# Optimization experiments

Measured on AMD Instinct MI355X. Metric: run time of the kernel, lower is better.

Reference implementation:

```python
import jax, jax.numpy as jnp
import numpy as np
from jax import lax

IN_FEATURES = 1024
CLASSES = 512
OUT_CHANNELS = 32
N = 4096
CONV1_OUT = 32
K = 3


def setup_inputs() -> dict:
    key = jax.random.key(0)
    ks = jax.random.split(key, 7)
    s_lin = 1.0 / np.sqrt(IN_FEATURES)
    s_c1 = 1.0 / np.sqrt(1 * K)
    s_c2 = 1.0 / np.sqrt(CONV1_OUT * K)
    return {
        "x": jax.random.normal(ks[0], (N, IN_FEATURES), dtype=jnp.float32),
        "W_w": jax.random.uniform(ks[1], (CLASSES, IN_FEATURES), jnp.float32, -s_lin, s_lin),
        "W_b": jax.random.uniform(ks[2], (CLASSES,), jnp.float32, -s_lin, s_lin),
        "conv1_w": jax.random.uniform(ks[3], (CONV1_OUT, 1, K), jnp.float32, -s_c1, s_c1),
        "conv1_b": jax.random.uniform(ks[4], (CONV1_OUT,), jnp.float32, -s_c1, s_c1),
        "conv2_w": jax.random.uniform(ks[5], (OUT_CHANNELS, CONV1_OUT, K), jnp.float32, -s_c2, s_c2),
        "conv2_b": jax.random.uniform(ks[6], (OUT_CHANNELS,), jnp.float32, -s_c2, s_c2),
    }


def _conv1d(x, w, b):
    # x: [N, C_in, L], w: [C_out, C_in, K], padding=1 (same)
    y = lax.conv_general_dilated(
        x, w, window_strides=(1,), padding=((1, 1),),
        dimension_numbers=("NCH", "OIH", "NCH"))
    return y + b[None, :, None]


def reference(x, W_w, W_b, conv1_w, conv1_b, conv2_w, conv2_b):
    # SelfAttention: h = x W^T + b  -> [N, CLASSES]
    h = x @ W_w.T + W_b
    # attention = softmax(tanh(h h^T), dim=1)  -> [N, N]
    scores = jnp.tanh(h @ h.T)
    attn = jax.nn.softmax(scores, axis=1)
    a = jnp.tanh(attn @ h)                     # [N, CLASSES]
    a = jax.nn.relu(a)
    # unsqueeze(-1).permute(0,2,1): [N, CLASSES] -> [N, 1, CLASSES]
    z = a[:, None, :]
    z = jax.nn.relu(_conv1d(z, conv1_w, conv1_b))   # [N, 32, CLASSES]
    z = jax.nn.relu(_conv1d(z, conv2_w, conv2_b))   # [N, OUT_CHANNELS, CLASSES]
    return jnp.transpose(z, (0, 2, 1))              # [N, CLASSES, OUT_CHANNELS]
```

## Files before the change

### kernel.cpp

```cpp
#include <hip/hip_runtime.h>

typedef __bf16 bf16_t;
typedef __bf16 bf16x8 __attribute__((ext_vector_type(8)));
typedef __bf16 bf16x4v __attribute__((ext_vector_type(4)));
typedef __bf16 bf16x2 __attribute__((ext_vector_type(2)));
typedef float f32x4 __attribute__((ext_vector_type(4)));

__device__ __forceinline__ float tanh_fast(float x) {
  float a = fabsf(x);
  float e = __expf(-2.f * a);
  float t = (1.f - e) / (1.f + e);
  return copysignf(t, x);
}

__device__ __forceinline__ void gload16(const void* g, void* l) {
  __builtin_amdgcn_global_load_lds(
      (const __attribute__((address_space(1))) void*)g,
      (__attribute__((address_space(3))) void*)l, 16, 0, 0);
}

__global__ __launch_bounds__(256) void cast_all_k(const float* __restrict__ x,
                                                  const float* __restrict__ Ww,
                                                  const float* __restrict__ w2,
                                                  bf16_t* __restrict__ xb,
                                                  bf16_t* __restrict__ Wbf,
                                                  bf16_t* __restrict__ w2rg) {
  const int bid = blockIdx.x;
  const int tid = threadIdx.x;
  if (bid < 4096) {
    const int i = bid * 256 + tid;
    float4 v = ((const float4*)x)[i];
    bf16x4v o;
    o[0] = (bf16_t)v.x; o[1] = (bf16_t)v.y; o[2] = (bf16_t)v.z; o[3] = (bf16_t)v.w;
    ((bf16x4v*)xb)[i] = o;
  } else if (bid < 4608) {
    const int i = (bid - 4096) * 256 + tid;
    float4 v = ((const float4*)Ww)[i];
    bf16x4v o;
    o[0] = (bf16_t)v.x; o[1] = (bf16_t)v.y; o[2] = (bf16_t)v.z; o[3] = (bf16_t)v.w;
    ((bf16x4v*)Wbf)[i] = o;
  } else {
    for (int i = tid; i < 3072; i += 256) {
      int o = i / 96, rem = i % 96, c = rem / 3, kk = rem % 3;
      w2rg[kk * 1024 + o * 32 + c] = (bf16_t)w2[i];
    }
  }
}

#define BAR() __builtin_amdgcn_s_barrier()
#define WLG() asm volatile("s_waitcnt lgkmcnt(0)" ::: "memory")
#define RDA(b, am)                                                              \
  do {                                                                          \
    _Pragma("unroll") for (int j = 0; j < 4; ++j) {                             \
      afr[j][0] = *(const bf16x8*)(pA + (b)*16384 + (am)*4096 + j*1024);        \
      afr[j][1] = *(const bf16x8*)(pA + (b)*16384 + 8192 + (am)*4096 + j*1024); \
    }                                                                           \
  } while (0)
#define RDB(b, bn)                                                              \
  do {                                                                          \
    _Pragma("unroll") for (int jj = 0; jj < 2; ++jj) {                          \
      bfr[jj][0] = *(const bf16x8*)(pB + (b)*16384 + ((bn)*2+jj)*1024);         \
      bfr[jj][1] = *(const bf16x8*)(pB + (b)*16384 + 8192 + ((bn)*2+jj)*1024);  \
    }                                                                           \
  } while (0)
#define MM16(am, bn)                                                            \
  do {                                                                          \
    __builtin_amdgcn_s_setprio(1);                                              \
    _Pragma("unroll") for (int kk = 0; kk < 2; ++kk)                            \
    _Pragma("unroll") for (int j = 0; j < 4; ++j)                               \
    _Pragma("unroll") for (int jj = 0; jj < 2; ++jj)                            \
      acc[(am)*4+j][(bn)*2+jj] = __builtin_amdgcn_mfma_f32_16x16x32_bf16(       \
          afr[j][kk], bfr[jj][kk], acc[(am)*4+j][(bn)*2+jj], 0, 0, 0);          \
    __builtin_amdgcn_s_setprio(0);                                              \
  } while (0)
#define STGA(tile, half)                                                        \
  do {                                                                          \
    const bf16_t* s_ = Ag + (size_t)(half)*128*lda + (tile)*64;                 \
    char* d_ = lds_raw + (half)*32768 + ((tile)&1)*16384 + tid*16;              \
    gload16(s_, d_); gload16(s_ + 32, d_ + 8192);                               \
  } while (0)
#define STGB(tile, half)                                                        \
  do {                                                                          \
    const bf16_t* s_ = Bg + (size_t)(half)*128*ldb + (tile)*64;                 \
    char* d_ = lds_raw + 65536 + (half)*32768 + ((tile)&1)*16384 + tid*16;      \
    gload16(s_, d_); gload16(s_ + 32, d_ + 8192);                               \
  } while (0)

template <int EPI>
__global__ __launch_bounds__(512, 2) void gemm8_k(const bf16_t* __restrict__ A,
                                                  const bf16_t* __restrict__ Bt,
                                                  bf16_t* __restrict__ out,
                                                  float* __restrict__ psum,
                                                  int lda, int ldb, int ldc,
                                                  int Klen, size_t pstride) {
  __shared__ __attribute__((aligned(16))) char lds_raw[131072];
  const int tid = threadIdx.x;
  const int wid = tid >> 6, l = tid & 63;
  const int wm = wid >> 2, wn = wid & 3;
  const int lr = l & 15, lkq = l >> 4;
  const int bx = blockIdx.x, by = blockIdx.y;
  const size_t koff = (size_t)blockIdx.z * Klen;
  const int NI = Klen >> 7;

  const int srow = tid >> 2;
  const int scol = ((tid & 3) * 8) ^ (((tid >> 5) & 1) << 4);
  const bf16_t* Ag = A + (size_t)(by * 256 + srow) * lda + koff + scol;
  const bf16_t* Bg = Bt + (size_t)(bx * 256 + srow) * ldb + koff + scol;

  const int kby = (lkq * 16) ^ (((lr >> 3) & 1) << 5);
  const char* pA = lds_raw + wm * 32768 + lr * 64 + kby;
  const char* pB = lds_raw + 65536 + (wn >> 1) * 32768 + ((wn & 1) * 64 + lr) * 64 + kby;

  bf16x8 afr[4][2], bfr[2][2];
  f32x4 acc[8][4];
#pragma unroll
  for (int m = 0; m < 8; ++m)
#pragma unroll
    for (int n = 0; n < 4; ++n) acc[m][n] = (f32x4){0.f, 0.f, 0.f, 0.f};

  STGA(0, 0); STGA(0, 1); STGB(0, 0); STGB(0, 1); STGA(1, 0);

  for (int i = 0; i < NI; ++i) {
    const int t1 = 2 * i + 1, t2 = 2 * i + 2, t3 = 2 * i + 3;
    const bool more = (i + 1 < NI);
    asm volatile("s_waitcnt vmcnt(2)" ::: "memory");
    BAR();
    RDA(0, 0); RDB(0, 0);
    STGA(t1, 1);
    WLG(); MM16(0, 0); BAR();
    RDB(0, 1); STGB(t1, 0);
    BAR(); WLG(); MM16(0, 1); BAR();
    RDA(0, 1); STGB(t1, 1);
    BAR(); WLG(); MM16(1, 1); BAR();
    RDB(0, 0);
    if (more) STGA(t2, 0);
    BAR(); WLG(); MM16(1, 0); BAR();
    if (more) { asm volatile("s_waitcnt vmcnt(2)" ::: "memory"); }
    else      { asm volatile("s_waitcnt vmcnt(0)" ::: "memory"); }
    BAR();
    RDA(1, 0); RDB(1, 0);
    if (more) STGA(t2, 1);
    WLG(); MM16(0, 0); BAR();
    RDB(1, 1);
    if (more) STGB(t2, 0);
    BAR(); WLG(); MM16(0, 1); BAR();
    RDA(1, 1);
    if (more) STGB(t2, 1);
    BAR(); WLG(); MM16(1, 1); BAR();
    RDB(1, 0);
    if (more) STGA(t3, 0);
    BAR(); WLG(); MM16(1, 0); BAR();
  }

  if constexpr (EPI == 1) {
    float* ps = psum + (size_t)(bx * 4 + wn) * 4096;
#pragma unroll
    for (int mi = 0; mi < 8; ++mi) {
#pragma unroll
      for (int v = 0; v < 4; ++v) {
        const int row = by * 256 + wm * 128 + mi * 16 + lkq * 4 + v;
        float rs = 0.f;
#pragma unroll
        for (int ni = 0; ni < 4; ++ni) {
          const int col = bx * 256 + wn * 64 + ni * 16 + lr;
          float val = __expf(tanh_fast(acc[mi][ni][v]));
          out[(size_t)row * ldc + col] = (bf16_t)val;
          rs += val;
        }
        rs += __shfl_xor(rs, 1);
        rs += __shfl_xor(rs, 2);
        rs += __shfl_xor(rs, 4);
        rs += __shfl_xor(rs, 8);
        if (lr == 0) ps[row] = rs;
      }
    }
  } else {
    bf16_t* o = out + (size_t)blockIdx.z * pstride;
#pragma unroll
    for (int mi = 0; mi < 8; ++mi)
#pragma unroll
      for (int v = 0; v < 4; ++v) {
        const int row = by * 256 + wm * 128 + mi * 16 + lkq * 4 + v;
#pragma unroll
        for (int ni = 0; ni < 4; ++ni)
          o[(size_t)row * ldc + bx * 256 + wn * 64 + ni * 16 + lr] = (bf16_t)acc[mi][ni][v];
      }
  }
}

template <int EPI>
__global__ __launch_bounds__(256) void gemm_bt_k(const bf16_t* __restrict__ A,
                                                 const bf16_t* __restrict__ Bt,
                                                 const float* __restrict__ extra,
                                                 bf16_t* __restrict__ out,
                                                 float* __restrict__ outf,
                                                 float* __restrict__ psum,
                                                 int M, int N, int Kloop, int lda, int ldb) {
  __shared__ bf16_t As[128 * 32];
  __shared__ bf16_t Bs[128 * 32];
  const int tid = threadIdx.x;
  const int w = tid >> 6;
  const int l = tid & 63;
  const int bx = blockIdx.x, by = blockIdx.y;
  const int koff = blockIdx.z * Kloop;

  const bf16_t* src = (w < 2) ? A : Bt;
  const int stride = (w < 2) ? lda : ldb;
  bf16_t* dstbase = (w < 2) ? As : Bs;
  const int tile0 = (w < 2 ? by : bx) * 128 + (w & 1) * 64;
  const int srow = l >> 2;
  const int scol = (l & 3) * 8;
  const bf16_t* gbase = src + (size_t)(tile0 + srow) * stride + scol + koff;
  bf16_t* lbase = dstbase + (w & 1) * (64 * 32);

  const int wm = w >> 1, wn = w & 1;
  const int lrow = l & 15;
  const int lk = (l >> 4) * 8;

  f32x4 zero = {0.f, 0.f, 0.f, 0.f};
  f32x4 acc[4][4];
  for (int m = 0; m < 4; ++m)
    for (int n = 0; n < 4; ++n) acc[m][n] = zero;

  for (int kt = 0; kt < Kloop; kt += 32) {
    const bf16_t* g = gbase + kt;
#pragma unroll
    for (int i = 0; i < 4; ++i) gload16(g + (size_t)i * 16 * stride, lbase + i * 512);
    __syncthreads();
    bf16x8 af[4], bfv[4];
#pragma unroll
    for (int m = 0; m < 4; ++m)
      af[m] = *(const bf16x8*)&As[(wm * 64 + m * 16 + lrow) * 32 + lk];
#pragma unroll
    for (int n = 0; n < 4; ++n)
      bfv[n] = *(const bf16x8*)&Bs[(wn * 64 + n * 16 + lrow) * 32 + lk];
#pragma unroll
    for (int m = 0; m < 4; ++m)
#pragma unroll
      for (int n = 0; n < 4; ++n)
        acc[m][n] = __builtin_amdgcn_mfma_f32_16x16x32_bf16(af[m], bfv[n], acc[m][n], 0, 0, 0);
    __syncthreads();
  }

  const int row0 = by * 128 + wm * 64;
  const int col0 = bx * 128 + wn * 64;

  if constexpr (EPI == 3) {
    float* of = outf + (size_t)blockIdx.z * M * N;
#pragma unroll
    for (int m = 0; m < 4; ++m)
#pragma unroll
      for (int v = 0; v < 4; ++v) {
        const int row = row0 + m * 16 + ((l >> 4) << 2) + v;
#pragma unroll
        for (int n = 0; n < 4; ++n)
          of[(size_t)row * N + col0 + n * 16 + lrow] = acc[m][n][v];
      }
    return;
  }

  if constexpr (EPI == 1) {
#pragma unroll
    for (int m = 0; m < 4; ++m)
#pragma unroll
      for (int v = 0; v < 4; ++v) {
        const int row = row0 + m * 16 + ((l >> 4) << 2) + v;
        float rs = 0.f;
#pragma unroll
        for (int n = 0; n < 4; ++n) {
          const int col = col0 + n * 16 + lrow;
          float val = __expf(tanh_fast(acc[m][n][v]));
          out[(size_t)row * N + col] = (bf16_t)val;
          rs += val;
        }
        if (psum) {
          rs += __shfl_xor(rs, 1);
          rs += __shfl_xor(rs, 2);
          rs += __shfl_xor(rs, 4);
          rs += __shfl_xor(rs, 8);
          if ((l & 15) == 0) psum[(size_t)(bx * 2 + wn) * M + row] = rs;
        }
      }
    return;
  }

  float bcol[4];
#pragma unroll
  for (int n = 0; n < 4; ++n)
    bcol[n] = (EPI == 0) ? extra[col0 + n * 16 + lrow] : 0.f;

#pragma unroll
  for (int m = 0; m < 4; ++m) {
#pragma unroll
    for (int v = 0; v < 4; ++v) {
      const int row = row0 + m * 16 + ((l >> 4) << 2) + v;
      float inv_dn = 1.f;
      if constexpr (EPI == 2) inv_dn = 1.f / extra[row];
#pragma unroll
      for (int n = 0; n < 4; ++n) {
        const int col = col0 + n * 16 + lrow;
        float val = acc[m][n][v];
        float o;
        if constexpr (EPI == 0) o = val + bcol[n];
        else o = fmaxf(tanh_fast(val * inv_dn), 0.f);
        out[(size_t)row * N + col] = (bf16_t)o;
      }
    }
  }
}

__global__ __launch_bounds__(256) void reduce1T_k(const float* __restrict__ p0,
                                                  const float* __restrict__ p1,
                                                  const float* __restrict__ bias,
                                                  bf16_t* __restrict__ h,
                                                  bf16_t* __restrict__ hT) {
  __shared__ bf16_t tile[64][65];
  const int d0 = blockIdx.x * 64;
  const int i0 = blockIdx.y * 64;
  const int tid = threadIdx.x;
#pragma unroll
  for (int p = 0; p < 2; ++p) {
    const int r = p * 32 + (tid >> 3);
    const int c8 = (tid & 7) * 8;
    const size_t idx = (size_t)(i0 + r) * 512 + d0 + c8;
    float4 a0 = *(const float4*)&p0[idx];
    float4 a1 = *(const float4*)&p0[idx + 4];
    float4 b0 = *(const float4*)&p1[idx];
    float4 b1 = *(const float4*)&p1[idx + 4];
    float4 w0 = *(const float4*)&bias[d0 + c8];
    float4 w1 = *(const float4*)&bias[d0 + c8 + 4];
    bf16x8 o;
    o[0] = (bf16_t)(a0.x + b0.x + w0.x);
    o[1] = (bf16_t)(a0.y + b0.y + w0.y);
    o[2] = (bf16_t)(a0.z + b0.z + w0.z);
    o[3] = (bf16_t)(a0.w + b0.w + w0.w);
    o[4] = (bf16_t)(a1.x + b1.x + w1.x);
    o[5] = (bf16_t)(a1.y + b1.y + w1.y);
    o[6] = (bf16_t)(a1.z + b1.z + w1.z);
    o[7] = (bf16_t)(a1.w + b1.w + w1.w);
    *(bf16x8*)&h[idx] = o;
#pragma unroll
    for (int k = 0; k < 8; ++k) tile[r][c8 + k] = o[k];
  }
  __syncthreads();
#pragma unroll
  for (int p = 0; p < 2; ++p) {
    const int d = p * 32 + (tid >> 3);
    const int i8 = (tid & 7) * 8;
    bf16x8 u;
#pragma unroll
    for (int k = 0; k < 8; ++k) u[k] = tile[i8 + k][d];
    *(bf16x8*)&hT[(size_t)(d0 + d) * 4096 + i0 + i8] = u;
  }
}

__global__ __launch_bounds__(256) void transpose_k(const bf16_t* __restrict__ h,
                                                   bf16_t* __restrict__ hT) {
  __shared__ bf16_t tile[64][65];
  const int i0 = blockIdx.x * 64;
  const int d0 = blockIdx.y * 64;
  const int tid = threadIdx.x;
#pragma unroll
  for (int p = 0; p < 2; ++p) {
    int r = p * 32 + (tid >> 3);
    int c8 = (tid & 7) * 8;
    bf16x8 v = *(const bf16x8*)&h[(size_t)(i0 + r) * 512 + d0 + c8];
#pragma unroll
    for (int k = 0; k < 8; ++k) tile[r][c8 + k] = v[k];
  }
  __syncthreads();
#pragma unroll
  for (int p = 0; p < 2; ++p) {
    int d = p * 32 + (tid >> 3);
    int i8 = (tid & 7) * 8;
    bf16x8 u;
#pragma unroll
    for (int k = 0; k < 8; ++k) u[k] = tile[i8 + k][d];
    *(bf16x8*)&hT[(size_t)(d0 + d) * 4096 + i0 + i8] = u;
  }
}

__global__ __launch_bounds__(256) void rowsum_k(const bf16_t* __restrict__ P,
                                                float* __restrict__ den) {
  const int r = blockIdx.x;
  const int tid = threadIdx.x;
  const bf16_t* p = P + (size_t)r * 4096 + tid * 16;
  bf16x8 a = *(const bf16x8*)p;
  bf16x8 b = *(const bf16x8*)(p + 8);
  float s = 0.f;
#pragma unroll
  for (int k = 0; k < 8; ++k) s += (float)a[k] + (float)b[k];
  __shared__ float red[256];
  red[tid] = s;
  __syncthreads();
  for (int off = 128; off > 0; off >>= 1) {
    if (tid < off) red[tid] += red[tid + off];
    __syncthreads();
  }
  if (tid == 0) den[r] = red[0];
}

__global__ __launch_bounds__(256) void conv2_fused_k(const bf16_t* __restrict__ pg,
                                                     const float* __restrict__ psum,
                                                     const bf16_t* __restrict__ w2rg,
                                                     const float* __restrict__ w1,
                                                     const float* __restrict__ b1,
                                                     const float* __restrict__ b2,
                                                     float* __restrict__ out, int S) {
  __shared__ bf16_t trow[516];
  __shared__ bf16_t z1t[514 * 40];
  __shared__ bf16_t w2r[3072];
  __shared__ float w1s[96], b1s[32], b2s[32];
  __shared__ float den_s;
  const int r = blockIdx.x;
  const int tid = threadIdx.x;

  if (tid < 96) w1s[tid] = w1[tid];
  if (tid < 32) { b1s[tid] = b1[tid]; b2s[tid] = b2[tid]; }
  ((bf16x8*)w2r)[tid] = ((const bf16x8*)w2rg)[tid];
  if (tid < 128) ((bf16x8*)w2r)[256 + tid] = ((const bf16x8*)w2rg)[256 + tid];

  if (tid < 64) {
    float dp = psum[(size_t)tid * 4096 + r];
    dp += __shfl_xor(dp, 32);
    dp += __shfl_xor(dp, 16);
    dp += __shfl_xor(dp, 8);
    dp += __shfl_xor(dp, 4);
    dp += __shfl_xor(dp, 2);
    dp += __shfl_xor(dp, 1);
    if (tid == 0) den_s = dp;
  }

  float a0 = 0.f, a1 = 0.f;
  {
    const bf16_t* pr = pg + (size_t)r * 512 + tid * 2;
    for (int z = 0; z < S; ++z) {
      bf16x2 v = *(const bf16x2*)(pr + (size_t)z * (4096 * 512));
      a0 += (float)v[0];
      a1 += (float)v[1];
    }
  }
  if (tid == 0) { trow[0] = (bf16_t)0.f; trow[513] = (bf16_t)0.f; }
  if (tid < 40) { z1t[tid] = (bf16_t)0.f; z1t[513 * 40 + tid] = (bf16_t)0.f; }
  __syncthreads();

  {
    const float inv = 1.f / den_s;
    trow[1 + 2 * tid] = (bf16_t)fmaxf(tanh_fast(a0 * inv), 0.f);
    trow[2 + 2 * tid] = (bf16_t)fmaxf(tanh_fast(a1 * inv), 0.f);
  }
  __syncthreads();

  {
    const int c = tid & 31;
    const int jb = (tid >> 5) * 64;
    const float wc0 = w1s[c * 3], wc1 = w1s[c * 3 + 1], wc2 = w1s[c * 3 + 2];
    const float bb = b1s[c];
    float tm = (float)trow[jb];
    float t0 = (float)trow[jb + 1];
    for (int j = jb; j < jb + 64; ++j) {
      float tp2 = (float)trow[j + 2];
      float v = fmaxf(bb + wc0 * tm + wc1 * t0 + wc2 * tp2, 0.f);
      z1t[(j + 1) * 40 + c] = (bf16_t)v;
      tm = t0; t0 = tp2;
    }
  }
  __syncthreads();

  const int w = tid >> 6, l = tid & 63;
  const int lrow = l & 15;
  const int lk = (l >> 4) * 8;
  bf16x8 af[3][2];
#pragma unroll
  for (int kk = 0; kk < 3; ++kk)
#pragma unroll
    for (int m = 0; m < 2; ++m)
      af[kk][m] = *(const bf16x8*)&w2r[kk * 1024 + (m * 16 + lrow) * 32 + lk];

  f32x4 zero = {0.f, 0.f, 0.f, 0.f};
  f32x4 acc[2][8];
#pragma unroll
  for (int m = 0; m < 2; ++m)
#pragma unroll
    for (int n = 0; n < 8; ++n) acc[m][n] = zero;

  const int j0 = w * 128;
#pragma unroll
  for (int kk = 0; kk < 3; ++kk) {
#pragma unroll
    for (int n = 0; n < 8; ++n) {
      bf16x8 bfv = *(const bf16x8*)&z1t[(j0 + n * 16 + lrow + kk) * 40 + lk];
      acc[0][n] = __builtin_amdgcn_mfma_f32_16x16x32_bf16(af[kk][0], bfv, acc[0][n], 0, 0, 0);
      acc[1][n] = __builtin_amdgcn_mfma_f32_16x16x32_bf16(af[kk][1], bfv, acc[1][n], 0, 0, 0);
    }
  }

#pragma unroll
  for (int m = 0; m < 2; ++m) {
    const int ob = m * 16 + ((l >> 4) << 2);
    const float bb0 = b2s[ob], bb1 = b2s[ob + 1], bb2 = b2s[ob + 2], bb3 = b2s[ob + 3];
#pragma unroll
    for (int n = 0; n < 8; ++n) {
      const int j = j0 + n * 16 + lrow;
      f32x4 res;
      res[0] = fmaxf(acc[m][n][0] + bb0, 0.f);
      res[1] = fmaxf(acc[m][n][1] + bb1, 0.f);
      res[2] = fmaxf(acc[m][n][2] + bb2, 0.f);
      res[3] = fmaxf(acc[m][n][3] + bb3, 0.f);
      *(f32x4*)&out[((size_t)r * 512 + j) * 32 + ob] = res;
    }
  }
}

__global__ __launch_bounds__(256) void conv_fused_k(const bf16_t* __restrict__ t,
                                                    const float* __restrict__ w1,
                                                    const float* __restrict__ b1,
                                                    const float* __restrict__ w2,
                                                    const float* __restrict__ b2,
                                                    float* __restrict__ out) {
  __shared__ bf16_t trow[516];
  __shared__ bf16_t z1t[514 * 40];
  __shared__ bf16_t w2r[3 * 32 * 32];
  __shared__ float w1s[96], b1s[32], b2s[32];
  const int r = blockIdx.x;
  const int tid = threadIdx.x;

  if (tid < 96) w1s[tid] = w1[tid];
  if (tid < 32) { b1s[tid] = b1[tid]; b2s[tid] = b2[tid]; }
  for (int i = tid; i < 3072; i += 256) {
    int o = i / 96, rem = i % 96, c = rem / 3, kk = rem % 3;
    w2r[kk * 1024 + o * 32 + c] = (bf16_t)w2[i];
  }
  {
    const bf16_t* tp = t + (size_t)r * 512;
    trow[1 + tid] = tp[tid];
    trow[1 + 256 + tid] = tp[256 + tid];
    if (tid == 0) { trow[0] = (bf16_t)0.f; trow[513] = (bf16_t)0.f; }
    if (tid < 40) { z1t[tid] = (bf16_t)0.f; z1t[513 * 40 + tid] = (bf16_t)0.f; }
  }
  __syncthreads();

  {
    const int c = tid & 31;
    const int jb = (tid >> 5) * 64;
    const float wc0 = w1s[c * 3], wc1 = w1s[c * 3 + 1], wc2 = w1s[c * 3 + 2];
    const float bb = b1s[c];
    float tm = (float)trow[jb];
    float t0 = (float)trow[jb + 1];
    for (int j = jb; j < jb + 64; ++j) {
      float tp2 = (float)trow[j + 2];
      float v = fmaxf(bb + wc0 * tm + wc1 * t0 + wc2 * tp2, 0.f);
      z1t[(j + 1) * 40 + c] = (bf16_t)v;
      tm = t0; t0 = tp2;
    }
  }
  __syncthreads();

  const int w = tid >> 6, l = tid & 63;
  const int lrow = l & 15;
  const int lk = (l >> 4) * 8;
  bf16x8 af[3][2];
#pragma unroll
  for (int kk = 0; kk < 3; ++kk)
#pragma unroll
    for (int m = 0; m < 2; ++m)
      af[kk][m] = *(const bf16x8*)&w2r[kk * 1024 + (m * 16 + lrow) * 32 + lk];

  f32x4 zero = {0.f, 0.f, 0.f, 0.f};
  f32x4 acc[2][8];
#pragma unroll
  for (int m = 0; m < 2; ++m)
#pragma unroll
    for (int n = 0; n < 8; ++n) acc[m][n] = zero;

  const int j0 = w * 128;
#pragma unroll
  for (int kk = 0; kk < 3; ++kk) {
#pragma unroll
    for (int n = 0; n < 8; ++n) {
      bf16x8 bfv = *(const bf16x8*)&z1t[(j0 + n * 16 + lrow + kk) * 40 + lk];
      acc[0][n] = __builtin_amdgcn_mfma_f32_16x16x32_bf16(af[kk][0], bfv, acc[0][n], 0, 0, 0);
      acc[1][n] = __builtin_amdgcn_mfma_f32_16x16x32_bf16(af[kk][1], bfv, acc[1][n], 0, 0, 0);
    }
  }

#pragma unroll
  for (int m = 0; m < 2; ++m) {
    const int ob = m * 16 + ((l >> 4) << 2);
    const float bb0 = b2s[ob], bb1 = b2s[ob + 1], bb2 = b2s[ob + 2], bb3 = b2s[ob + 3];
#pragma unroll
    for (int n = 0; n < 8; ++n) {
      const int j = j0 + n * 16 + lrow;
      f32x4 res;
      res[0] = fmaxf(acc[m][n][0] + bb0, 0.f);
      res[1] = fmaxf(acc[m][n][1] + bb1, 0.f);
      res[2] = fmaxf(acc[m][n][2] + bb2, 0.f);
      res[3] = fmaxf(acc[m][n][3] + bb3, 0.f);
      *(f32x4*)&out[((size_t)r * 512 + j) * 32 + ob] = res;
    }
  }
}

extern "C" void kernel_launch(void* const* d_in, const int* in_sizes, int n_in,
                              void* d_out, int out_size, void* d_ws, size_t ws_size,
                              hipStream_t stream) {
  const float* x = (const float*)d_in[0];
  const float* Ww = (const float*)d_in[1];
  const float* Wb = (const float*)d_in[2];
  const float* c1w = (const float*)d_in[3];
  const float* c1b = (const float*)d_in[4];
  const float* c2w = (const float*)d_in[5];
  const float* c2b = (const float*)d_in[6];
  float* out = (float*)d_out;
  char* ws = (char*)d_ws;

  bf16_t* xb  = (bf16_t*)(ws + 0);
  bf16_t* Wbf = (bf16_t*)(ws + 8388608);
  bf16_t* h   = (bf16_t*)(ws + 9437184);
  bf16_t* hT  = (bf16_t*)(ws + 13631488);
  bf16_t* tb  = (bf16_t*)(ws + 17825792);
  bf16_t* w2rg = (bf16_t*)(ws + 17825792);
  float*  den = (float*)(ws + 22020096);

  cast_all_k<<<4609, 256, 0, stream>>>(x, Ww, c2w, xb, Wbf, w2rg);

  const size_t NEED_FAST = 73416704ull;
  if (ws_size >= NEED_FAST) {
    float*  psum = (float*)(ws + 22036480);
    bf16_t* P    = (bf16_t*)(ws + 23085056);
    float*  pg1  = (float*)(ws + 23085056);
    bf16_t* pg3b = (bf16_t*)(ws + 56639488);

    gemm_bt_k<3><<<dim3(4, 32, 2), 256, 0, stream>>>(xb, Wbf, nullptr, nullptr, pg1,
                                                     nullptr, 4096, 512, 512, 1024, 1024);
    reduce1T_k<<<dim3(8, 64), 256, 0, stream>>>(pg1, pg1 + 4096 * 512, Wb, h, hT);

    gemm8_k<1><<<dim3(16, 16, 1), 512, 0, stream>>>(h, h, P, psum, 512, 512, 4096, 512, 0);

    const int S = (ws_size >= 90193920ull) ? 8 : 4;
    gemm8_k<3><<<dim3(2, 16, S), 512, 0, stream>>>(P, hT, pg3b, nullptr, 4096, 4096, 512,
                                                   4096 / S, (size_t)4096 * 512);

    conv2_fused_k<<<4096, 256, 0, stream>>>(pg3b, psum, w2rg, c1w, c1b, c2b, out, S);
  } else {
    bf16_t* P = (bf16_t*)(ws + 22036480);
    gemm_bt_k<0><<<dim3(4, 32), 256, 0, stream>>>(xb, Wbf, Wb, h, nullptr, nullptr,
                                                  4096, 512, 1024, 1024, 1024);
    transpose_k<<<dim3(64, 8), 256, 0, stream>>>(h, hT);
    gemm_bt_k<1><<<dim3(32, 32), 256, 0, stream>>>(h, h, nullptr, P, nullptr, nullptr,
                                                   4096, 4096, 512, 512, 512);
    rowsum_k<<<4096, 256, 0, stream>>>(P, den);
    gemm_bt_k<2><<<dim3(4, 32), 256, 0, stream>>>(P, hT, den, tb, nullptr, nullptr,
                                                  4096, 512, 4096, 4096, 4096);
    conv_fused_k<<<4096, 256, 0, stream>>>(tb, c1w, c1b, c2w, c2b, out);
  }
}
```

Baseline: 184.8 us.

## Stage GEMM epilogue through LDS for 16-byte stores, swizzle block order

The 256x256 output tile is now written to LDS with an XOR swizzle and then copied out to global memory as coalesced 16-byte vector stores, replacing scattered 2-byte stores. The block index is also remapped so consecutive launched blocks are spread in strides of one eighth of the grid, which changes which tiles are resident together and how they share the L2/MALL caches. The tanh division becomes a hardware reciprocal. The epilogue needs one more barrier, the remap assumes power-of-two grid dimensions, and the reciprocal gives up some accuracy.

```diff
diff --git a/kernel.cpp b/kernel.cpp
--- a/kernel.cpp
+++ b/kernel.cpp
@@ -9,7 +9,7 @@
 __device__ __forceinline__ float tanh_fast(float x) {
   float a = fabsf(x);
   float e = __expf(-2.f * a);
-  float t = (1.f - e) / (1.f + e);
+  float t = (1.f - e) * __builtin_amdgcn_rcpf(1.f + e);
   return copysignf(t, x);
 }
 
@@ -98,8 +98,17 @@
   const int wid = tid >> 6, l = tid & 63;
   const int wm = wid >> 2, wn = wid & 3;
   const int lr = l & 15, lkq = l >> 4;
-  const int bx = blockIdx.x, by = blockIdx.y;
-  const size_t koff = (size_t)blockIdx.z * Klen;
+
+  const int gx = gridDim.x, gy = gridDim.y;
+  const int flat = blockIdx.x + gx * (blockIdx.y + gy * blockIdx.z);
+  const int n = gx * gy * gridDim.z;
+  const int s = (flat & 7) * (n >> 3) + (flat >> 3);
+  const int lgx = __builtin_ctz(gx), lgy = __builtin_ctz(gy);
+  const int bx = s & (gx - 1);
+  const int by = (s >> lgx) & (gy - 1);
+  const int bz = s >> (lgx + lgy);
+
+  const size_t koff = (size_t)bz * Klen;
   const int NI = Klen >> 7;
 
   const int srow = tid >> 2;
@@ -116,7 +125,7 @@
 #pragma unroll
   for (int m = 0; m < 8; ++m)
 #pragma unroll
-    for (int n = 0; n < 4; ++n) acc[m][n] = (f32x4){0.f, 0.f, 0.f, 0.f};
+    for (int n2 = 0; n2 < 4; ++n2) acc[m][n2] = (f32x4){0.f, 0.f, 0.f, 0.f};
 
   STGA(0, 0); STGA(0, 1); STGB(0, 0); STGB(0, 1); STGA(1, 0);
 
@@ -158,33 +167,43 @@
     for (int mi = 0; mi < 8; ++mi) {
 #pragma unroll
       for (int v = 0; v < 4; ++v) {
-        const int row = by * 256 + wm * 128 + mi * 16 + lkq * 4 + v;
+        const int r = wm * 128 + mi * 16 + lkq * 4 + v;
         float rs = 0.f;
 #pragma unroll
         for (int ni = 0; ni < 4; ++ni) {
-          const int col = bx * 256 + wn * 64 + ni * 16 + lr;
           float val = __expf(tanh_fast(acc[mi][ni][v]));
-          out[(size_t)row * ldc + col] = (bf16_t)val;
+          const int cb = ((wn * 64 + ni * 16 + lr) * 2) ^ ((r & 4) << 4);
+          *(bf16_t*)(lds_raw + r * 512 + cb) = (bf16_t)val;
           rs += val;
         }
         rs += __shfl_xor(rs, 1);
         rs += __shfl_xor(rs, 2);
         rs += __shfl_xor(rs, 4);
         rs += __shfl_xor(rs, 8);
-        if (lr == 0) ps[row] = rs;
+        if (lr == 0) ps[by * 256 + r] = rs;
       }
     }
   } else {
-    bf16_t* o = out + (size_t)blockIdx.z * pstride;
 #pragma unroll
     for (int mi = 0; mi < 8; ++mi)
 #pragma unroll
       for (int v = 0; v < 4; ++v) {
-        const int row = by * 256 + wm * 128 + mi * 16 + lkq * 4 + v;
-#pragma unroll
-        for (int ni = 0; ni < 4; ++ni)
-          o[(size_t)row * ldc + bx * 256 + wn * 64 + ni * 16 + lr] = (bf16_t)acc[mi][ni][v];
+        const int r = wm * 128 + mi * 16 + lkq * 4 + v;
+#pragma unroll
+        for (int ni = 0; ni < 4; ++ni) {
+          const int cb = ((wn * 64 + ni * 16 + lr) * 2) ^ ((r & 4) << 4);
+          *(bf16_t*)(lds_raw + r * 512 + cb) = (bf16_t)acc[mi][ni][v];
+        }
       }
+  }
+  __syncthreads();
+  bf16_t* obase = (EPI == 1) ? out : out + (size_t)bz * pstride;
+#pragma unroll
+  for (int k = 0; k < 16; ++k) {
+    const int idx = k * 512 + tid;
+    const int row = idx >> 5, cc = idx & 31;
+    bf16x8 vv = *(const bf16x8*)(lds_raw + ((row * 512 + cc * 16) ^ ((row & 4) << 4)));
+    *(bf16x8*)&obase[(size_t)(by * 256 + row) * ldc + bx * 256 + cc * 8] = vv;
   }
 }
 
```

New measurement: 182.9 us. No clear change (-1.0%).
